# Kernel optimization log

Measured on AMD Instinct MI355X. Metric: run time of the kernel, lower is better.

Reference implementation:

```python
import jax, jax.numpy as jnp
import numpy as np

B, T, D, H, L, OUT, FC = 256, 512, 64, 256, 2, 1, 128


def setup_inputs() -> dict:
    key = jax.random.key(0)
    ks = jax.random.split(key, 16)
    s = 1.0 / np.sqrt(H)
    u = lambda k, shape: jax.random.uniform(k, shape, jnp.float32, -s, s)
    return {
        "x": jax.random.normal(ks[0], (B, T, D), jnp.float32),
        # layer 0 LSTM params (PyTorch gate order: i, f, g, o)
        "W_ih0": u(ks[1], (4 * H, D)),
        "W_hh0": u(ks[2], (4 * H, H)),
        "b_ih0": u(ks[3], (4 * H,)),
        "b_hh0": u(ks[4], (4 * H,)),
        # layer 1 LSTM params
        "W_ih1": u(ks[5], (4 * H, H)),
        "W_hh1": u(ks[6], (4 * H, H)),
        "b_ih1": u(ks[7], (4 * H,)),
        "b_hh1": u(ks[8], (4 * H,)),
        # MLP head
        "fc1_w": u(ks[9], (FC, H)),
        "fc1_b": u(ks[10], (FC,)),
        "fc2_w": u(ks[11], (OUT, FC)),
        "fc2_b": u(ks[12], (OUT,)),
    }


def _lstm_layer(x, W_ih, W_hh, b_ih, b_hh):
    # x: [B, T, Din] -> (outputs [B, T, H], final hidden [B, H])
    Bsz = x.shape[0]
    Hh = W_hh.shape[1]
    # precompute input contribution to all gates: [B, T, 4H]
    xg = jnp.einsum("btd,gd->btg", x, W_ih) + b_ih + b_hh

    def step(carry, xt):
        h, c = carry
        g = xt + h @ W_hh.T  # [B, 4H]
        i, f, gg, o = jnp.split(g, 4, axis=-1)
        i = jax.nn.sigmoid(i)
        f = jax.nn.sigmoid(f)
        gg = jnp.tanh(gg)
        o = jax.nn.sigmoid(o)
        c = f * c + i * gg
        h = o * jnp.tanh(c)
        return (h, c), h

    h0 = jnp.zeros((Bsz, Hh), x.dtype)
    (hT, _cT), hs = jax.lax.scan(step, (h0, h0), jnp.swapaxes(xg, 0, 1))
    return jnp.swapaxes(hs, 0, 1), hT


def reference(x, W_ih0, W_hh0, b_ih0, b_hh0, W_ih1, W_hh1, b_ih1, b_hh1,
              fc1_w, fc1_b, fc2_w, fc2_b):
    # eval-mode forward: inter-layer dropout (p=0.2) is a no-op
    y0, h0f = _lstm_layer(x, W_ih0, W_hh0, b_ih0, b_hh0)
    _y1, h1f = _lstm_layer(y0, W_ih1, W_hh1, b_ih1, b_hh1)
    # h_n.view(-1, H): stack per-layer final hidden states -> [L*B, H]
    h_n = jnp.concatenate([h0f, h1f], axis=0)
    out = jax.nn.relu(h_n)
    out = jax.nn.relu(out @ fc1_w.T + fc1_b)
    return out @ fc2_w.T + fc2_b  # [L*B, OUT]
```

## Files before the change

kernel.cpp:

```cpp
#include <hip/hip_runtime.h>

#define Bb 256
#define Tt 512
#define Dd 64
#define Hh 256
#define NP 16
#define HB2 (256 * 256)
#define FSTRIDE 16

typedef unsigned short u16;
typedef _Float16 f16;
typedef __attribute__((ext_vector_type(8))) _Float16 f16x8;
typedef __attribute__((ext_vector_type(4))) _Float16 f16x4;
typedef __attribute__((ext_vector_type(4))) float f32x4;
typedef __attribute__((ext_vector_type(4))) unsigned int u32x4;

__device__ __forceinline__ f16x8 bc8h(u32x4 v) { return __builtin_bit_cast(f16x8, v); }

__device__ __forceinline__ float fsig(float x) {
  x = fminf(fmaxf(x, -30.f), 30.f);
  return 1.f / (1.f + __expf(-x));
}
__device__ __forceinline__ float ftanh(float x) {
  x = fminf(fmaxf(x, -15.f), 15.f);
  float t = __expf(2.f * x);
  return (t - 1.f) / (t + 1.f);
}

__device__ __forceinline__ f16x8 ld16_sc1(const f16* p) {
  f16x8 r;
  asm volatile("global_load_dwordx4 %0, %1, off sc1" : "=v"(r) : "v"(p) : "memory");
  return r;
}
__device__ __forceinline__ f16x8 ld16_sc0(const f16* p) {
  f16x8 r;
  asm volatile("global_load_dwordx4 %0, %1, off sc0" : "=v"(r) : "v"(p) : "memory");
  return r;
}
__device__ __forceinline__ void st2_sc1(f16* p, unsigned v) {
  asm volatile("global_store_short %0, %1, off sc1" : : "v"(p), "v"(v) : "memory");
}
__device__ __forceinline__ void st2_plain(f16* p, unsigned v) {
  asm volatile("global_store_short %0, %1, off" : : "v"(p), "v"(v) : "memory");
}
__device__ __forceinline__ void st4u_plain(unsigned* p, unsigned v) {
  asm volatile("global_store_dword %0, %1, off" : : "v"(p), "v"(v) : "memory");
}
__device__ __forceinline__ void st4u_sc1(unsigned* p, unsigned v) {
  asm volatile("global_store_dword %0, %1, off sc1" : : "v"(p), "v"(v) : "memory");
}
__device__ __forceinline__ unsigned ld4_sc0(const unsigned* p) {
  unsigned r;
  asm volatile("global_load_dword %0, %1, off sc0\n\ts_waitcnt vmcnt(0)"
               : "=v"(r) : "v"(p) : "memory");
  return r;
}
__device__ __forceinline__ void atomswap_l2(unsigned* p, unsigned v) {
  asm volatile("global_atomic_swap %0, %1, off" : : "v"(p), "v"(v) : "memory");
}
__device__ __forceinline__ void atomadd_l2(unsigned* p, unsigned v) {
  asm volatile("global_atomic_add %0, %1, off" : : "v"(p), "v"(v) : "memory");
}
__device__ __forceinline__ unsigned atomadd0_l2(unsigned* p) {
  unsigned r;
  asm volatile("global_atomic_add %0, %1, %2, off sc0\n\ts_waitcnt vmcnt(0)"
               : "=v"(r) : "v"(p), "v"(0u) : "memory");
  return r;
}

__global__ __launch_bounds__(256) void prep_x(const float* __restrict__ x,
                                              f16* __restrict__ xh) {
  int i = blockIdx.x * blockDim.x + threadIdx.x;
  const int n4 = Bb * Tt * Dd / 4;
  if (i >= n4) return;
  f32x4 v = ((const f32x4*)x)[i];
  f16x4 o;
#pragma unroll
  for (int j = 0; j < 4; ++j) o[j] = (f16)v[j];
  ((f16x4*)xh)[i] = o;
}

__global__ __launch_bounds__(256) void prep_w(
    const float* __restrict__ wih0, const float* __restrict__ whh0,
    const float* __restrict__ bih0, const float* __restrict__ bhh0,
    const float* __restrict__ wih1, const float* __restrict__ whh1,
    const float* __restrict__ bih1, const float* __restrict__ bhh1,
    f16* __restrict__ wfrag, float* __restrict__ bias0s, float* __restrict__ bias1s) {
  int tid = blockIdx.x * blockDim.x + threadIdx.x;
  int np = gridDim.x * blockDim.x;
  const int tot = 16 * 8 * 32 * 512;
  for (int u = tid; u < tot; u += np) {
    int e = u & 7, l = (u >> 3) & 63;
    int f = (u >> 9) & 31;
    int wv = (u >> 14) & 7;
    int p = u >> 17;
    int g = wv & 3;
    int grow = g * 256 + p * 16 + (l & 15);
    int klane = (l >> 4) * 8 + e;
    float w = 0.f;
    if (wv < 4) {
      if (f < 4)       w = wih0[grow * 64 + (f >> 1) * 32 + klane];
      else if (f < 20) w = whh0[grow * 256 + ((f - 4) >> 1) * 32 + klane];
    } else {
      if (f < 16)      w = wih1[grow * 256 + (f >> 1) * 32 + klane];
      else             w = whh1[grow * 256 + ((f - 16) >> 1) * 32 + klane];
    }
    f16 hi = (f16)w;
    wfrag[u] = (f & 1) ? (f16)((w - (float)hi) * 2048.0f) : hi;
  }
  for (int u = tid; u < 1024; u += np) {
    bias0s[u] = bih0[u] + bhh0[u];
    bias1s[u] = bih1[u] + bhh1[u];
  }
}

#define MF(A, B, C) __builtin_amdgcn_mfma_f32_16x16x32_f16(A, B, C, 0, 0, 0)

__global__ __launch_bounds__(512, 1) void lstm_persist(
    const f16* __restrict__ xh, const f16* __restrict__ wfrag,
    const float* __restrict__ bias0s, const float* __restrict__ bias1s,
    f16* h0, f16* h1, unsigned* flagcnt, unsigned* probe, unsigned* verdict) {
  const int bid = blockIdx.x;
  const int p = (bid >> 3) & 15;
  const int grp = (bid & 7) * 2 + (bid >> 7);
  const int tid = threadIdx.x;
  const int wv = tid >> 6, lane = tid & 63;
  const int lr = lane & 15, lk = lane >> 4;
  const int g = wv & 3;
  const bool isL1 = wv >= 4;
  const float LOSCALE = 1.0f / 2048.0f;

  __shared__ float gbuf[2][4][16][16];
  __shared__ u32x4 hbuf[2][16][36];
  __shared__ unsigned s_fast;
  __shared__ int s_mbox;

  if (tid == 0) s_mbox = -1;

  f16x8 wf[32];
  {
    const u32x4* wp = (const u32x4*)wfrag + ((size_t)(p * 8 + wv) * 32) * 64 + lane;
#pragma unroll
    for (int f = 0; f < 20; ++f) wf[f] = bc8h(wp[(size_t)f * 64]);
    if (isL1) {
#pragma unroll
      for (int f = 20; f < 32; ++f) wf[f] = bc8h(wp[(size_t)f * 64]);
    }
  }
  const float bias = (isL1 ? bias1s : bias0s)[g * 256 + p * 16 + lr];

  if (tid < 256) {
    int lsel = tid >> 7;
    int d = tid & 127;
    int row = d >> 3, cp = d & 7;
    f16* base = lsel ? h1 : (h0 + (size_t)3 * HB2);
    unsigned* w = (unsigned*)(base + (size_t)(grp * 16 + row) * 256 + p * 16) + cp;
    st4u_plain(w, 0u);
    st4u_sc1(w, 0u);
  }
  if (tid == 0) {
    atomswap_l2(&flagcnt[(grp * NP + p) * FSTRIDE], 0u);
    __hip_atomic_store(&flagcnt[(grp * NP + p) * FSTRIDE], 0u, __ATOMIC_RELAXED,
                       __HIP_MEMORY_SCOPE_AGENT);
  }
  asm volatile("s_waitcnt vmcnt(0)" ::: "memory");
  __syncthreads();

  if (wv == 0) {
    if (lane == 0) {
      st4u_plain(&probe[grp * NP + p], (unsigned)(p + 1));
      asm volatile("s_waitcnt vmcnt(0)" ::: "memory");
    }
    bool seen = (lane >= NP);
    bool ok;
    int it = 0;
    while (true) {
      if (!seen) {
        unsigned got = ld4_sc0(&probe[grp * NP + lane]);
        if (got == (unsigned)(lane + 1)) seen = true;
      }
      if (__all(seen)) { ok = true; break; }
      if (++it > 768) { ok = false; break; }
      __builtin_amdgcn_s_sleep(2);
    }
    if (lane == 0)
      __hip_atomic_store(&verdict[grp * NP + p], ok ? 1u : 2u, __ATOMIC_RELAXED,
                         __HIP_MEMORY_SCOPE_AGENT);
    unsigned v;
    while (true) {
      v = 1u;
      if (lane < NP)
        v = __hip_atomic_load(&verdict[grp * NP + lane], __ATOMIC_RELAXED,
                              __HIP_MEMORY_SCOPE_AGENT);
      if (!__any(v == 0u)) break;
      __builtin_amdgcn_s_sleep(2);
    }
    if (lane == 0) s_fast = __any(v != 1u) ? 0u : 1u;
  }
  __syncthreads();
  const bool fast = (s_fast != 0u);

  const int eL = tid >> 8;
  const int erow = (tid >> 4) & 15, ecol = tid & 15;
  float c = 0.f;
  f16* const hout = ((eL ? h1 : h0) + (size_t)(grp * 16 + erow) * 256 + p * 16 + ecol);

  const int hrow = grp * 16 + lr;
  const f16* xbase = xh + (size_t)hrow * Tt * Dd + lk * 8;
  const f16* hsrcbase = ((wv < 4) ? h0 : h1) + (size_t)grp * 4096;
  const int hlsel = wv >> 2;
  unsigned* const mycnt = &flagcnt[(grp * NP + p) * FSTRIDE];

  for (int k = 0; k <= Tt; ++k) {
    f32x4 a = (f32x4){bias, bias, bias, bias};
    f32x4 b = (f32x4){0.f, 0.f, 0.f, 0.f};
    if (!isL1 && k < Tt) {
      const u32x4* xp = (const u32x4*)(xbase + (size_t)k * Dd);
      f16x8 xf0 = bc8h(xp[0]);
      f16x8 xf1 = bc8h(xp[4]);
      a = MF(xf0, wf[0], a);
      b = MF(xf0, wf[1], b);
      a = MF(xf1, wf[2], a);
      b = MF(xf1, wf[3], b);
    }

    if (wv == 0) {
      const unsigned thr = 8u * (unsigned)k;
      int it = 0;
      bool ready = false;
      while (!ready) {
        unsigned v = 0xFFFFFFFFu;
        if (lane < NP) {
          if (fast)
            v = atomadd0_l2(&flagcnt[(grp * NP + lane) * FSTRIDE]);
          else
            v = __hip_atomic_load(&flagcnt[(grp * NP + lane) * FSTRIDE],
                                  __ATOMIC_RELAXED, __HIP_MEMORY_SCOPE_AGENT);
        }
        ready = !__any(v < thr);
        if (!ready) {
          if (++it > 65536) break;
          __builtin_amdgcn_s_sleep(1);
        }
      }
      __hip_atomic_store(&s_mbox, k, __ATOMIC_RELAXED,
                         __HIP_MEMORY_SCOPE_WORKGROUP);
    } else {
      while (__hip_atomic_load(&s_mbox, __ATOMIC_RELAXED,
                               __HIP_MEMORY_SCOPE_WORKGROUP) < k)
        __builtin_amdgcn_s_sleep(1);
    }
    asm volatile("" ::: "memory");

    const int par = (k - 1) & 3;

    {
      const f16* src = hsrcbase + (size_t)par * HB2;
      const int j0 = (wv & 3) * 2;
      const f16* p0 = src + j0 * 512 + lane * 8;
      f16x8 s0, s1;
      if (fast) {
        s0 = ld16_sc0(p0);
        s1 = ld16_sc0(p0 + 512);
      } else {
        s0 = ld16_sc1(p0);
        s1 = ld16_sc1(p0 + 512);
      }
      asm volatile("s_waitcnt vmcnt(0)" ::: "memory");
      const int r0 = j0 * 2 + (lane >> 5);
      const int c2 = lane & 31;
      hbuf[hlsel][r0][c2 ^ (r0 & 7)] = __builtin_bit_cast(u32x4, s0);
      hbuf[hlsel][r0 + 2][c2 ^ ((r0 + 2) & 7)] = __builtin_bit_cast(u32x4, s1);
    }
    __syncthreads();

    f16x8 A0[8], A1[8];
#pragma unroll
    for (int kt = 0; kt < 8; ++kt)
      A0[kt] = __builtin_bit_cast(f16x8, hbuf[0][lr][(kt * 4 + lk) ^ (lr & 7)]);
    if (isL1) {
#pragma unroll
      for (int kt = 0; kt < 8; ++kt)
        A1[kt] = __builtin_bit_cast(f16x8, hbuf[1][lr][(kt * 4 + lk) ^ (lr & 7)]);
    }

    if (!isL1) {
      if (k < Tt) {
#pragma unroll
        for (int kt = 0; kt < 8; ++kt) {
          a = MF(A0[kt], wf[4 + 2 * kt], a);
          b = MF(A0[kt], wf[5 + 2 * kt], b);
        }
        a += b * LOSCALE;
#pragma unroll
        for (int r = 0; r < 4; ++r) gbuf[0][g][lk * 4 + r][lr] = a[r];
      }
    } else if (k >= 1) {
#pragma unroll
      for (int kt = 0; kt < 8; ++kt) {
        a = MF(A0[kt], wf[2 * kt], a);
        b = MF(A0[kt], wf[2 * kt + 1], b);
      }
#pragma unroll
      for (int kt = 0; kt < 8; ++kt) {
        a = MF(A1[kt], wf[16 + 2 * kt], a);
        b = MF(A1[kt], wf[17 + 2 * kt], b);
      }
      a += b * LOSCALE;
#pragma unroll
      for (int r = 0; r < 4; ++r) gbuf[1][g][lk * 4 + r][lr] = a[r];
    }
    __syncthreads();

    {
      const bool upd = eL ? (k >= 1) : (k < Tt);
      if (upd) {
        float iv = fsig(gbuf[eL][0][erow][ecol]);
        float fv = fsig(gbuf[eL][1][erow][ecol]);
        float gv = ftanh(gbuf[eL][2][erow][ecol]);
        float ov = fsig(gbuf[eL][3][erow][ecol]);
        c = fv * c + iv * gv;
        float hval = ov * ftanh(c);
        f16 fh = (f16)hval;
        unsigned bits = (unsigned)__builtin_bit_cast(u16, fh);
        f16* Ho = hout + (size_t)(k & 3) * HB2;
        if (fast) st2_plain(Ho, bits);
        else      st2_sc1(Ho, bits);
      }
    }
    asm volatile("s_waitcnt vmcnt(0)" ::: "memory");
    if (lane == 0) {
      if (fast) atomadd_l2(mycnt, 1u);
      else (void)__hip_atomic_fetch_add(mycnt, 1u, __ATOMIC_RELAXED,
                                        __HIP_MEMORY_SCOPE_AGENT);
    }
  }
}

__global__ __launch_bounds__(128) void head_kernel(
    const f16* __restrict__ h0f, const f16* __restrict__ h1f,
    const float* __restrict__ fc1w, const float* __restrict__ fc1b,
    const float* __restrict__ fc2w, const float* __restrict__ fc2b,
    float* __restrict__ out) {
  int r = blockIdx.x;
  const f16* hh = (r < 256) ? (h0f + r * Hh) : (h1f + (r - 256) * Hh);
  __shared__ float v[Hh];
  int tid = threadIdx.x;
  for (int i = tid; i < Hh; i += 128)
    v[i] = fmaxf((float)hh[i], 0.f);
  __syncthreads();
  float s = fc1b[tid];
#pragma unroll 8
  for (int i = 0; i < Hh; ++i) s += fc1w[tid * Hh + i] * v[i];
  s = fmaxf(s, 0.f) * fc2w[tid];
#pragma unroll
  for (int off = 32; off; off >>= 1) s += __shfl_down(s, off);
  __shared__ float red[2];
  if ((tid & 63) == 0) red[tid >> 6] = s;
  __syncthreads();
  if (tid == 0) out[r] = red[0] + red[1] + fc2b[0];
}

extern "C" void kernel_launch(void* const* d_in, const int* in_sizes, int n_in,
                              void* d_out, int out_size, void* d_ws, size_t ws_size,
                              hipStream_t stream) {
  (void)in_sizes; (void)n_in; (void)out_size; (void)ws_size;
  const float* x    = (const float*)d_in[0];
  const float* wih0 = (const float*)d_in[1];
  const float* whh0 = (const float*)d_in[2];
  const float* bih0 = (const float*)d_in[3];
  const float* bhh0 = (const float*)d_in[4];
  const float* wih1 = (const float*)d_in[5];
  const float* whh1 = (const float*)d_in[6];
  const float* bih1 = (const float*)d_in[7];
  const float* bhh1 = (const float*)d_in[8];
  const float* fc1w = (const float*)d_in[9];
  const float* fc1b = (const float*)d_in[10];
  const float* fc2w = (const float*)d_in[11];
  const float* fc2b = (const float*)d_in[12];

  char* ws = (char*)d_ws;
  size_t off = 0;
  f16* xh = (f16*)(ws + off); off += (size_t)Bb * Tt * Dd * 2;
  f16* wfrag = (f16*)(ws + off); off += (size_t)16 * 8 * 32 * 512 * 2;
  float* bias0s = (float*)(ws + off); off += 4096;
  float* bias1s = (float*)(ws + off); off += 4096;
  char* zbase = ws + off;
  f16* h0 = (f16*)(ws + off); off += (size_t)4 * HB2 * 2;
  f16* h1 = (f16*)(ws + off); off += (size_t)4 * HB2 * 2;
  unsigned* flagcnt = (unsigned*)(ws + off); off += 256 * FSTRIDE * 4;
  unsigned* probe = (unsigned*)(ws + off); off += 1024;
  unsigned* verdict = (unsigned*)(ws + off); off += 1024;
  size_t zbytes = (size_t)((ws + off) - zbase);

  hipMemsetAsync(zbase, 0, zbytes, stream);
  prep_x<<<Bb * Tt * Dd / 4 / 256, 256, 0, stream>>>(x, xh);
  prep_w<<<512, 256, 0, stream>>>(wih0, whh0, bih0, bhh0, wih1, whh1, bih1, bhh1,
                                  wfrag, bias0s, bias1s);
  lstm_persist<<<256, 512, 0, stream>>>(xh, wfrag, bias0s, bias1s, h0, h1,
                                        flagcnt, probe, verdict);
  head_kernel<<<512, 128, 0, stream>>>(h0 + (size_t)3 * HB2, h1, fc1w, fc1b,
                                       fc2w, fc2b, (float*)d_out);
}
```

Before: 1.425 ms.

## Permute gate rows so each wave holds all four gates and drop the LDS gate exchange

Reorders the weight fragment rows so that each wave's 16 MFMA output columns cover the i,f,g,o gates for 4 hidden units. A 4x4 transpose through register shuffles then gives every lane its own four gate values, which removes the shared-memory gate buffer and one block-wide barrier per timestep. The mailbox spin-wait also drops its s_sleep, trading busier polling for lower wake-up latency. This adds cross-lane shuffles and ties the weight layout, bias indexing and output addressing together, so any mismatch among them would silently corrupt results.

```diff
diff --git a/kernel.cpp b/kernel.cpp
--- a/kernel.cpp
+++ b/kernel.cpp
@@ -94,8 +94,8 @@
     int f = (u >> 9) & 31;
     int wv = (u >> 14) & 7;
     int p = u >> 17;
-    int g = wv & 3;
-    int grow = g * 256 + p * 16 + (l & 15);
+    int cc = l & 15;
+    int grow = (cc >> 2) * 256 + p * 16 + (wv & 3) * 4 + (cc & 3);
     int klane = (l >> 4) * 8 + e;
     float w = 0.f;
     if (wv < 4) {
@@ -130,7 +130,6 @@
   const bool isL1 = wv >= 4;
   const float LOSCALE = 1.0f / 2048.0f;
 
-  __shared__ float gbuf[2][4][16][16];
   __shared__ u32x4 hbuf[2][16][36];
   __shared__ unsigned s_fast;
   __shared__ int s_mbox;
@@ -147,7 +146,8 @@
       for (int f = 20; f < 32; ++f) wf[f] = bc8h(wp[(size_t)f * 64]);
     }
   }
-  const float bias = (isL1 ? bias1s : bias0s)[g * 256 + p * 16 + lr];
+  const float bias =
+      (isL1 ? bias1s : bias0s)[(lr >> 2) * 256 + p * 16 + g * 4 + (lr & 3)];
 
   if (tid < 256) {
     int lsel = tid >> 7;
@@ -200,10 +200,10 @@
   __syncthreads();
   const bool fast = (s_fast != 0u);
 
-  const int eL = tid >> 8;
-  const int erow = (tid >> 4) & 15, ecol = tid & 15;
+  const int xj = lane & 3, jj = (lane >> 2) & 3;
   float c = 0.f;
-  f16* const hout = ((eL ? h1 : h0) + (size_t)(grp * 16 + erow) * 256 + p * 16 + ecol);
+  f16* const hout = (isL1 ? h1 : h0) +
+                    (size_t)(grp * 16 + lk * 4 + jj) * 256 + p * 16 + g * 4 + xj;
 
   const int hrow = grp * 16 + lr;
   const f16* xbase = xh + (size_t)hrow * Tt * Dd + lk * 8;
@@ -247,8 +247,8 @@
                          __HIP_MEMORY_SCOPE_WORKGROUP);
     } else {
       while (__hip_atomic_load(&s_mbox, __ATOMIC_RELAXED,
-                               __HIP_MEMORY_SCOPE_WORKGROUP) < k)
-        __builtin_amdgcn_s_sleep(1);
+                               __HIP_MEMORY_SCOPE_WORKGROUP) < k) {
+      }
     }
     asm volatile("" ::: "memory");
 
@@ -284,18 +284,16 @@
         A1[kt] = __builtin_bit_cast(f16x8, hbuf[1][lr][(kt * 4 + lk) ^ (lr & 7)]);
     }
 
+    const bool upd = isL1 ? (k >= 1) : (k < Tt);
     if (!isL1) {
-      if (k < Tt) {
+      if (upd) {
 #pragma unroll
         for (int kt = 0; kt < 8; ++kt) {
           a = MF(A0[kt], wf[4 + 2 * kt], a);
           b = MF(A0[kt], wf[5 + 2 * kt], b);
         }
-        a += b * LOSCALE;
-#pragma unroll
-        for (int r = 0; r < 4; ++r) gbuf[0][g][lk * 4 + r][lr] = a[r];
-      }
-    } else if (k >= 1) {
+      }
+    } else if (upd) {
 #pragma unroll
       for (int kt = 0; kt < 8; ++kt) {
         a = MF(A0[kt], wf[2 * kt], a);
@@ -306,27 +304,36 @@
         a = MF(A1[kt], wf[16 + 2 * kt], a);
         b = MF(A1[kt], wf[17 + 2 * kt], b);
       }
-      a += b * LOSCALE;
-#pragma unroll
-      for (int r = 0; r < 4; ++r) gbuf[1][g][lk * 4 + r][lr] = a[r];
-    }
-    __syncthreads();
-
-    {
-      const bool upd = eL ? (k >= 1) : (k < Tt);
-      if (upd) {
-        float iv = fsig(gbuf[eL][0][erow][ecol]);
-        float fv = fsig(gbuf[eL][1][erow][ecol]);
-        float gv = ftanh(gbuf[eL][2][erow][ecol]);
-        float ov = fsig(gbuf[eL][3][erow][ecol]);
-        c = fv * c + iv * gv;
-        float hval = ov * ftanh(c);
-        f16 fh = (f16)hval;
-        unsigned bits = (unsigned)__builtin_bit_cast(u16, fh);
-        f16* Ho = hout + (size_t)(k & 3) * HB2;
-        if (fast) st2_plain(Ho, bits);
-        else      st2_sc1(Ho, bits);
-      }
+    }
+
+    if (upd) {
+      f32x4 v = a + b * LOSCALE;
+      const int s0b = (lane >> 2) & 1, s1b = (lane >> 3) & 1;
+      {
+        float e0 = s1b ? v[0] : v[2];
+        float e1 = s1b ? v[1] : v[3];
+        float f0 = __shfl_xor(e0, 8);
+        float f1 = __shfl_xor(e1, 8);
+        if (s1b) { v[0] = f0; v[1] = f1; } else { v[2] = f0; v[3] = f1; }
+      }
+      {
+        float g0 = s0b ? v[0] : v[1];
+        float g1 = s0b ? v[2] : v[3];
+        float h0v = __shfl_xor(g0, 4);
+        float h1v = __shfl_xor(g1, 4);
+        if (s0b) { v[0] = h0v; v[2] = h1v; } else { v[1] = h0v; v[3] = h1v; }
+      }
+      float iv = fsig(v[0]);
+      float fv = fsig(v[1]);
+      float gv = ftanh(v[2]);
+      float ov = fsig(v[3]);
+      c = fv * c + iv * gv;
+      float hval = ov * ftanh(c);
+      f16 fh = (f16)hval;
+      unsigned bits = (unsigned)__builtin_bit_cast(u16, fh);
+      f16* Ho = hout + (size_t)(k & 3) * HB2;
+      if (fast) st2_plain(Ho, bits);
+      else      st2_sc1(Ho, bits);
     }
     asm volatile("s_waitcnt vmcnt(0)" ::: "memory");
     if (lane == 0) {
```

New measurement: 1.946 ms. +36.6%, slower.

## Offload wave 0 gate update to wave 1 and overlap x-MFMA with h loads

Applied to the files above, without the earlier changes.

Wave 0 polls the cross-block step flags every timestep. Its share of the LSTM elementwise gate update is moved to wave 1, which now computes two cells per lane, so wave 0 can return to polling sooner. The input-projection MFMAs are issued after the global loads of the previous hidden state, so they overlap that load latency. The other waves also spin on the LDS mailbox without s_sleep, which cuts wake-up delay but keeps their SIMDs busy while they wait. Wave 1 now carries twice the transcendental work, which lengthens its own per-step critical path.

```diff
diff --git a/kernel.cpp b/kernel.cpp
--- a/kernel.cpp
+++ b/kernel.cpp
@@ -202,27 +202,28 @@
 
   const int eL = tid >> 8;
   const int erow = (tid >> 4) & 15, ecol = tid & 15;
-  float c = 0.f;
+  const bool hasOwn = (wv != 0);
+  const bool hasExtra = (wv == 1);
+  float c = 0.f, c2 = 0.f;
   f16* const hout = ((eL ? h1 : h0) + (size_t)(grp * 16 + erow) * 256 + p * 16 + ecol);
-
-  const int hrow = grp * 16 + lr;
-  const f16* xbase = xh + (size_t)hrow * Tt * Dd + lk * 8;
+  f16* const hout2 =
+      h0 + (size_t)(grp * 16 + (lane >> 4)) * 256 + p * 16 + (lane & 15);
+
+  const f16* xbase = xh + (size_t)(grp * 16 + lr) * Tt * Dd + lk * 8;
   const f16* hsrcbase = ((wv < 4) ? h0 : h1) + (size_t)grp * 4096;
   const int hlsel = wv >> 2;
   unsigned* const mycnt = &flagcnt[(grp * NP + p) * FSTRIDE];
 
   for (int k = 0; k <= Tt; ++k) {
+    f16x8 xf0, xf1;
+    const bool havex = (!isL1 && k < Tt);
+    if (havex) {
+      const u32x4* xp = (const u32x4*)(xbase + (size_t)k * Dd);
+      xf0 = bc8h(xp[0]);
+      xf1 = bc8h(xp[4]);
+    }
     f32x4 a = (f32x4){bias, bias, bias, bias};
     f32x4 b = (f32x4){0.f, 0.f, 0.f, 0.f};
-    if (!isL1 && k < Tt) {
-      const u32x4* xp = (const u32x4*)(xbase + (size_t)k * Dd);
-      f16x8 xf0 = bc8h(xp[0]);
-      f16x8 xf1 = bc8h(xp[4]);
-      a = MF(xf0, wf[0], a);
-      b = MF(xf0, wf[1], b);
-      a = MF(xf1, wf[2], a);
-      b = MF(xf1, wf[3], b);
-    }
 
     if (wv == 0) {
       const unsigned thr = 8u * (unsigned)k;
@@ -247,8 +248,8 @@
                          __HIP_MEMORY_SCOPE_WORKGROUP);
     } else {
       while (__hip_atomic_load(&s_mbox, __ATOMIC_RELAXED,
-                               __HIP_MEMORY_SCOPE_WORKGROUP) < k)
-        __builtin_amdgcn_s_sleep(1);
+                               __HIP_MEMORY_SCOPE_WORKGROUP) < k) {
+      }
     }
     asm volatile("" ::: "memory");
 
@@ -266,11 +267,17 @@
         s0 = ld16_sc1(p0);
         s1 = ld16_sc1(p0 + 512);
       }
+      if (havex) {
+        a = MF(xf0, wf[0], a);
+        b = MF(xf0, wf[1], b);
+        a = MF(xf1, wf[2], a);
+        b = MF(xf1, wf[3], b);
+      }
       asm volatile("s_waitcnt vmcnt(0)" ::: "memory");
       const int r0 = j0 * 2 + (lane >> 5);
-      const int c2 = lane & 31;
-      hbuf[hlsel][r0][c2 ^ (r0 & 7)] = __builtin_bit_cast(u32x4, s0);
-      hbuf[hlsel][r0 + 2][c2 ^ ((r0 + 2) & 7)] = __builtin_bit_cast(u32x4, s1);
+      const int c2i = lane & 31;
+      hbuf[hlsel][r0][c2i ^ (r0 & 7)] = __builtin_bit_cast(u32x4, s0);
+      hbuf[hlsel][r0 + 2][c2i ^ ((r0 + 2) & 7)] = __builtin_bit_cast(u32x4, s1);
     }
     __syncthreads();
 
@@ -312,9 +319,9 @@
     }
     __syncthreads();
 
-    {
-      const bool upd = eL ? (k >= 1) : (k < Tt);
-      if (upd) {
+    if (hasOwn) {
+      const bool updOwn = eL ? (k >= 1) : (k < Tt);
+      if (updOwn) {
         float iv = fsig(gbuf[eL][0][erow][ecol]);
         float fv = fsig(gbuf[eL][1][erow][ecol]);
         float gv = ftanh(gbuf[eL][2][erow][ecol]);
@@ -324,6 +331,20 @@
         f16 fh = (f16)hval;
         unsigned bits = (unsigned)__builtin_bit_cast(u16, fh);
         f16* Ho = hout + (size_t)(k & 3) * HB2;
+        if (fast) st2_plain(Ho, bits);
+        else      st2_sc1(Ho, bits);
+      }
+      if (hasExtra && (k < Tt)) {
+        const int er2 = lane >> 4, ec2 = lane & 15;
+        float iv = fsig(gbuf[0][0][er2][ec2]);
+        float fv = fsig(gbuf[0][1][er2][ec2]);
+        float gv = ftanh(gbuf[0][2][er2][ec2]);
+        float ov = fsig(gbuf[0][3][er2][ec2]);
+        c2 = fv * c2 + iv * gv;
+        float hval = ov * ftanh(c2);
+        f16 fh = (f16)hval;
+        unsigned bits = (unsigned)__builtin_bit_cast(u16, fh);
+        f16* Ho = hout2 + (size_t)(k & 3) * HB2;
         if (fast) st2_plain(Ho, bits);
         else      st2_sc1(Ho, bits);
       }
```

New measurement: 2.429 ms. 1.7x slower.
